# Kernel tuning notes

Measured on AMD Instinct MI355X. Metric: run time of the kernel, lower is better.

The kernel has to match this reference:

```python
import jax, jax.numpy as jnp
import numpy as np
from jax import lax

Z_MAX = 0.3
WAVELENGTHS = jnp.array([0.65, 0.53, 0.47], jnp.float32)
LUMA = jnp.array([0.299, 0.587, 0.114], jnp.float32)


def conv2d(x, w, b):
    # x: (B,C,H,W), w: (O,I,kh,kw), SAME padding, stride 1
    y = lax.conv_general_dilated(x, w, (1, 1), 'SAME',
                                 dimension_numbers=('NCHW', 'OIHW', 'NCHW'))
    return y + b[None, :, None, None]


def group_norm(x, g, b, eps=1e-5):
    # GroupNorm(num_groups=1): normalize over (C,H,W) per sample
    mu = x.mean(axis=(1, 2, 3), keepdims=True)
    var = ((x - mu) ** 2).mean(axis=(1, 2, 3), keepdims=True)
    xn = (x - mu) * lax.rsqrt(var + eps)
    return xn * g[None, :, None, None] + b[None, :, None, None]


def setup_inputs() -> dict:
    key = jax.random.key(0)
    ks = jax.random.split(key, 16)
    B, C, H, W = 8, 3, 512, 512
    PH, ZH, MH = 16, 16, 32
    s = 0.1
    inp = {
        'x': jax.random.uniform(ks[0], (B, C, H, W), jnp.float32),
        'norm_g': jnp.ones((C,), jnp.float32), 'norm_b': jnp.zeros((C,), jnp.float32),
        'ph_w1': jax.random.normal(ks[1], (PH, C, 3, 3), jnp.float32) * s,
        'ph_b1': jnp.zeros((PH,), jnp.float32),
        'ph_w2': jax.random.normal(ks[2], (C, PH, 3, 3), jnp.float32) * s,
        'ph_b2': jnp.zeros((C,), jnp.float32),
        'z_w1': jax.random.normal(ks[3], (ZH, C, 3, 3), jnp.float32) * s,
        'z_b1': jnp.zeros((ZH,), jnp.float32),
        'z_w2': jax.random.normal(ks[4], (C, ZH, 3, 3), jnp.float32) * s,
        'z_b2': jnp.zeros((C,), jnp.float32),
        'freq_gain': jax.random.normal(ks[5], (C,), jnp.float32) * 0.01,
        'mix_w1': jax.random.normal(ks[6], (MH, C + 2, 3, 3), jnp.float32) * s,
        'mix_b1': jnp.zeros((MH,), jnp.float32),
        'gn1_g': jnp.ones((MH,), jnp.float32), 'gn1_b': jnp.zeros((MH,), jnp.float32),
        'mix_w2': jax.random.normal(ks[7], (MH, MH, 3, 3), jnp.float32) * s,
        'mix_b2': jnp.zeros((MH,), jnp.float32),
        'gn2_g': jnp.ones((MH,), jnp.float32), 'gn2_b': jnp.zeros((MH,), jnp.float32),
        'mix_w3': jax.random.normal(ks[8], (C, MH, 1, 1), jnp.float32) * s,
        'mix_b3': jnp.zeros((C,), jnp.float32),
        'se_w1': jax.random.normal(ks[9], (4, C), jnp.float32) * s,   # mid = max(3//4,4)=4
        'se_b1': jnp.zeros((4,), jnp.float32),
        'se_w2': jax.random.normal(ks[10], (C, 4), jnp.float32) * s,
        'se_b2': jnp.zeros((C,), jnp.float32),
        'alpha': jnp.asarray(0.3, jnp.float32),
    }
    return inp


def reference(x, norm_g, norm_b, ph_w1, ph_b1, ph_w2, ph_b2,
              z_w1, z_b1, z_w2, z_b2, freq_gain,
              mix_w1, mix_b1, gn1_g, gn1_b, mix_w2, mix_b2, gn2_g, gn2_b,
              mix_w3, mix_b3, se_w1, se_b1, se_w2, se_b2, alpha):
    B, C, H, W = x.shape
    # 1) norm
    xn = group_norm(x, norm_g, norm_b)
    # 2) phase prediction (small CNN, phi in [-pi, pi])
    h = jax.nn.silu(conv2d(xn, ph_w1, ph_b1))
    phi = jnp.tanh(conv2d(h, ph_w2, ph_b2)) * jnp.pi
    # 3) per-pixel propagation distance z in [0, z_max]
    hz = jax.nn.silu(conv2d(xn, z_w1, z_b1))
    z = jax.nn.sigmoid(conv2d(hz, z_w2, z_b2)) * Z_MAX
    # 4) complex field U0 = amp * exp(i*phi)  (amp_mode='identity')
    U0 = lax.complex(x * jnp.cos(phi), x * jnp.sin(phi))
    # 5) ASM propagation. kz = 2*pi*sqrt(1/lam^2 - fx^2 - fy^2), per-channel wavelength.
    fy = jnp.fft.fftfreq(H).astype(jnp.float32)
    fx = jnp.fft.fftfreq(W).astype(jnp.float32)
    f2 = fy[:, None] ** 2 + fx[None, :] ** 2                     # (H,W)
    inv_l2 = (1.0 / WAVELENGTHS ** 2)[:, None, None]             # (3,1,1)
    kz = 2.0 * jnp.pi * jnp.sqrt(jnp.maximum(inv_l2 - f2[None], 0.0))  # (3,H,W)
    # spatially varying z: base propagation at mean z + spatial phase correction
    z_mean = z.mean(axis=(2, 3), keepdims=True)                  # (B,3,1,1)
    Uf = jnp.fft.fft2(U0)
    Uf = Uf * (1.0 + freq_gain)[None, :, None, None].astype(Uf.dtype)  # FreqEnhance gain
    hp = kz[None] * z_mean                                       # (B,3,H,W)
    Uz = jnp.fft.ifft2(Uf * lax.complex(jnp.cos(hp), jnp.sin(hp)))
    k0 = (2.0 * jnp.pi / WAVELENGTHS)[None, :, None, None]
    cp = k0 * (z - z_mean)
    Uz = Uz * lax.complex(jnp.cos(cp), jnp.sin(cp))
    # 6) J = |Uz| with clamped sqrt
    J = jnp.sqrt(jnp.maximum(Uz.real ** 2 + Uz.imag ** 2, 1e-12))
    # 7) mix head: [x, J_luma, J_contrast] -> delta
    lw = LUMA[None, :, None, None]
    x_l = (x * lw).sum(axis=1, keepdims=True)
    J_l = (J * lw).sum(axis=1, keepdims=True)
    mix_in = jnp.concatenate([x, J_l, J_l - x_l], axis=1)        # (B,5,H,W)
    d = jax.nn.silu(group_norm(conv2d(mix_in, mix_w1, mix_b1), gn1_g, gn1_b))
    d = jax.nn.silu(group_norm(conv2d(d, mix_w2, mix_b2), gn2_g, gn2_b))
    delta = conv2d(d, mix_w3, mix_b3)                            # (B,3,H,W)
    # 8) SE channel attention
    p = delta.mean(axis=(2, 3))                                  # (B,3)
    wse = jax.nn.sigmoid(jax.nn.silu(p @ se_w1.T + se_b1) @ se_w2.T + se_b2)
    delta = delta * wse[:, :, None, None]
    # 9) residual update
    return x + alpha * delta
```

## Files before the change

### kernel.cpp

```cpp
#include <hip/hip_runtime.h>
#include <hip/hip_bf16.h>
#include <math.h>

#define DINL __device__ __forceinline__

namespace {
constexpr int Bn = 8, Cn = 3, Hn = 512, Wn = 512;
constexpr int HW  = Hn * Wn;
constexpr int CHW = Cn * HW;
constexpr float GEPS = 1e-5f;
constexpr float PIf  = 3.14159265358979323846f;

constexpr size_t OFF_RED = 0;
constexpr size_t OFF_PHI = 512;
constexpr size_t OFF_U   = OFF_PHI + (size_t)Bn * CHW * 2;
constexpr size_t OFF_J   = OFF_U   + (size_t)Bn * CHW * 4;
constexpr size_t OFF_D   = OFF_J   + (size_t)Bn * CHW * 2;
constexpr size_t OFF_Y2  = OFF_D   + (size_t)Bn * CHW * 2;
constexpr size_t OFF_W1B = OFF_Y2  + (size_t)Bn * 32 * HW;
constexpr size_t OFF_W2F = OFF_W1B + 3072 * 2;
constexpr size_t OFF_WH1 = OFF_W2F + 9216;
constexpr size_t OFF_WP2 = OFF_WH1 + 4608 * 2;
constexpr size_t OFF_WZ2 = OFF_WP2 + 4608;
constexpr size_t OFF_PRM = OFF_WZ2 + 4608;
constexpr size_t OFF_PART= OFF_PRM + 160 * 4;
constexpr size_t OFF_TW  = OFF_PART + 81920 * 4;
constexpr int PZ = 0;
constexpr int PG1 = 24576;
constexpr int PG2 = 40960;
constexpr int PD  = 57344;
}

typedef __bf16 bfx8 __attribute__((ext_vector_type(8)));
typedef float  fx4  __attribute__((ext_vector_type(4)));
typedef float  fx2  __attribute__((ext_vector_type(2)));

DINL float frcp(float a) { return __builtin_amdgcn_rcpf(a); }
DINL float sigm(float a) { return frcp(1.f + __expf(-a)); }
DINL float siluf(float a) { return a * frcp(1.f + __expf(-a)); }
DINL float ftanh(float a) { return 1.f - 2.f * frcp(1.f + __expf(2.f * a)); }
DINL unsigned short f2bf(float f) {
    unsigned u = __float_as_uint(f);
    return (unsigned short)((u + 0x7FFFu + ((u >> 16) & 1u)) >> 16);
}
DINL float bf2f(unsigned short h) {
    return __uint_as_float(((unsigned)h) << 16);
}
DINL unsigned short t1(float a) { return (unsigned short)(__float_as_uint(a) >> 16); }
DINL unsigned t2(float a, float b) {
    return (__float_as_uint(a) >> 16) | (__float_as_uint(b) & 0xFFFF0000u);
}
DINL unsigned char f2f8(float v) {
    return (unsigned char)(__builtin_amdgcn_cvt_pk_fp8_f32(v, v, 0, false) & 0xFF);
}
DINL unsigned short pk8(float a, float b) {
    return (unsigned short)(__builtin_amdgcn_cvt_pk_fp8_f32(a, b, 0, false) & 0xFFFF);
}
DINL unsigned pk4f8(float a, float b, float c, float d) {
    unsigned u = __builtin_amdgcn_cvt_pk_fp8_f32(a, b, 0, false);
    u = __builtin_amdgcn_cvt_pk_fp8_f32(c, d, u, true);
    return u;
}
template<int SEL>
DINL float f8f(unsigned u) { return __builtin_amdgcn_cvt_f32_fp8(u, SEL); }
DINL unsigned pkh(float a, float b) {
    auto h = __builtin_amdgcn_cvt_pkrtz(a, b);
    unsigned u; __builtin_memcpy(&u, &h, 4); return u;
}
DINL float2 uph(unsigned u) {
    _Float16 h[2]; __builtin_memcpy(h, &u, 4);
    return make_float2((float)h[0], (float)h[1]);
}
DINL unsigned short f2h(float a) {
    _Float16 h = (_Float16)a; unsigned short s; __builtin_memcpy(&s, &h, 2); return s;
}
DINL float h2f(unsigned short s) {
    _Float16 h; __builtin_memcpy(&h, &s, 2); return (float)h;
}

DINL int SW(int e) { return e ^ ((e >> 4) & 7); }

DINL float blockReduceSum(float v) {
    __shared__ float sm[4];
    int lane = threadIdx.x & 63, wid = threadIdx.x >> 6;
    #pragma unroll
    for (int o = 32; o > 0; o >>= 1) v += __shfl_down(v, o, 64);
    __syncthreads();
    if (lane == 0) sm[wid] = v;
    __syncthreads();
    if (wid == 0) {
        float r = (lane < 4) ? sm[lane] : 0.f;
        r += __shfl_down(r, 2, 64);
        r += __shfl_down(r, 1, 64);
        return r;
    }
    return 0.f;
}

DINL void blockReduceSum3(float& a, float& b, float& c) {
    __shared__ float sm3[12];
    int lane = threadIdx.x & 63, wid = threadIdx.x >> 6;
    #pragma unroll
    for (int o = 32; o > 0; o >>= 1) {
        a += __shfl_down(a, o, 64);
        b += __shfl_down(b, o, 64);
        c += __shfl_down(c, o, 64);
    }
    __syncthreads();
    if (lane == 0) { sm3[wid] = a; sm3[4 + wid] = b; sm3[8 + wid] = c; }
    __syncthreads();
    if (threadIdx.x == 0) {
        a = sm3[0] + sm3[1] + sm3[2] + sm3[3];
        b = sm3[4] + sm3[5] + sm3[6] + sm3[7];
        c = sm3[8] + sm3[9] + sm3[10] + sm3[11];
    }
}

__global__ __launch_bounds__(256) void k_init(
    const float* __restrict__ w1, const float* __restrict__ w2,
    const float* __restrict__ phw1, const float* __restrict__ zw1,
    const float* __restrict__ phw2, const float* __restrict__ zw2,
    const float* __restrict__ g2g, const float* __restrict__ g2b,
    const float* __restrict__ w3,
    unsigned short* __restrict__ w1bf, unsigned char* __restrict__ w2f8,
    unsigned short* __restrict__ wh1, unsigned char* __restrict__ wp2,
    unsigned char* __restrict__ wz2, float* __restrict__ prm,
    float2* __restrict__ gtw,
    const float* __restrict__ x, float* __restrict__ part)
{
    if (blockIdx.x < 36) {
        int i = blockIdx.x * 256 + threadIdx.x;
        if (i < 3072) {
            int o = i / 96, k = i - o * 96;
            int ky = k >> 5, r = k & 31, kx = r >> 3, c = r & 7;
            float v = (kx < 3 && c < 5) ? w1[o * 45 + c * 9 + ky * 3 + kx] : 0.f;
            w1bf[i] = f2bf(v);
        }
        if (i < 9216) {
            int tap = i >> 10, rr = i & 1023, o = rr >> 5, ci = rr & 31;
            w2f8[i] = f2f8(w2[o * 288 + ci * 9 + tap]);
        }
        if (i < 4608) {
            int o = i / 96, k = i - o * 96;
            int ky = k >> 5, r = k & 31, kx = r >> 3, c = r & 7;
            float v = 0.f;
            if (kx < 3 && c < 3)
                v = (o < 16) ? phw1[o * 27 + c * 9 + ky * 3 + kx]
                             : zw1[(o - 16) * 27 + c * 9 + ky * 3 + kx];
            wh1[i] = f2bf(v);
        }
        if (i < 4608) {
            int tap = i / 512, rr = i - tap * 512, n = rr >> 5, k = rr & 31;
            float vp = (n < 3 && k < 16) ? phw2[n * 144 + k * 9 + tap] : 0.f;
            float vz = (n < 3) ? zw2[n * 288 + k * 9 + tap] : 0.f;
            wp2[i] = f2f8(vp);
            wz2[i] = f2f8(vz);
        }
        if (i < 160) {
            if (i < 32) {
                int ch = (i & 1) * 16 + (i >> 1);
                prm[i] = g2g[ch];
            } else if (i < 64) {
                int j = i - 32, ch = (j & 1) * 16 + (j >> 1);
                prm[i] = g2b[ch];
            } else {
                int j = (i - 64) & 31, c = (i - 64) >> 5;
                int ch = (j & 1) * 16 + (j >> 1);
                prm[i] = w3[c * 32 + ch];
            }
        }
        return;
    }
    if (blockIdx.x == 36) {
        for (int i = threadIdx.x; i < 512; i += 256) {
            float s, c; __sincosf(-2.f * PIf * (float)i * (1.f / 512.f), &s, &c);
            gtw[i] = make_float2(c, s);
        }
        return;
    }
    const int bid = blockIdx.x - 37;
    const int b = bid >> 5, blk = bid & 31;
    const float4* xv = (const float4*)(x + (size_t)b * CHW + (size_t)blk * (CHW / 32));
    float s = 0.f, ss = 0.f;
    for (int i = threadIdx.x; i < (CHW / 32) / 4; i += 256) {
        float4 v = xv[i];
        s  += v.x + v.y + v.z + v.w;
        ss += v.x * v.x + v.y * v.y + v.z * v.z + v.w * v.w;
    }
    float rs = blockReduceSum(s);
    float rss = blockReduceSum(ss);
    if (threadIdx.x == 0) {
        part[PG1 + b * 64 + blk] = rs;
        part[PG1 + b * 64 + 32 + blk] = rss;
    }
}

__global__ __launch_bounds__(256) void k_heads(
    const float* __restrict__ x,
    const float* __restrict__ ng, const float* __restrict__ nb,
    const unsigned short* __restrict__ wh1,
    const float* __restrict__ phb1, const float* __restrict__ zb1,
    const unsigned char* __restrict__ wp2, const unsigned char* __restrict__ wz2,
    const float* __restrict__ phb2, const float* __restrict__ zb2,
    unsigned short* __restrict__ phi, float* __restrict__ part)
{
    const int tx0 = blockIdx.x * 16, ty0 = blockIdx.y * 16, b = blockIdx.z;
    const int local = blockIdx.y * 32 + blockIdx.x;
    const bool edge = (blockIdx.x == 0) || (blockIdx.x == 31) ||
                      (blockIdx.y == 0) || (blockIdx.y == 31);
    __shared__ unsigned short mt8[20 * 21 * 8];
    __shared__ __attribute__((aligned(16))) unsigned char ht8[324 * 48];
    __shared__ float xst[2];
    const int t = threadIdx.x;
    {
        const float* px = part + PG1 + (size_t)b * 64;
        float sv  = (t < 32) ? px[t] : 0.f;
        float ssv = (t >= 32 && t < 64) ? px[t] : 0.f;
        float r0 = blockReduceSum(sv);
        float r1 = blockReduceSum(ssv);
        if (t == 0) { xst[0] = r0; xst[1] = r1; }
        __syncthreads();
    }
    const float mu = xst[0] * (1.f / CHW);
    const float rsv = rsqrtf(xst[1] * (1.f / CHW) - mu * mu + GEPS);
    float sc[3], sh[3];
    #pragma unroll
    for (int c = 0; c < 3; ++c) { sc[c] = rsv * ng[c]; sh[c] = nb[c] - mu * rsv * ng[c]; }
    if (edge) {
        for (int e = t; e < 20 * 21; e += 256) {
            int yy = e / 21, xx = e - yy * 21;
            int gy = ty0 - 2 + yy, gx = tx0 - 2 + xx;
            float v0 = 0, v1 = 0, v2 = 0;
            if (xx < 20 && (unsigned)gy < (unsigned)Hn && (unsigned)gx < (unsigned)Wn) {
                size_t p = (size_t)b * CHW + (size_t)gy * Wn + gx;
                v0 = x[p] * sc[0] + sh[0];
                v1 = x[p + HW] * sc[1] + sh[1];
                v2 = x[p + 2 * HW] * sc[2] + sh[2];
            }
            *(uint4*)(mt8 + e * 8) = make_uint4(t2(v0, v1), (unsigned)t1(v2), 0u, 0u);
        }
    } else {
        for (int e = t; e < 20 * 21; e += 256) {
            int yy = e / 21, xx = e - yy * 21;
            float v0 = 0, v1 = 0, v2 = 0;
            if (xx < 20) {
                size_t p = (size_t)b * CHW + (size_t)(ty0 - 2 + yy) * Wn + (tx0 - 2 + xx);
                v0 = x[p] * sc[0] + sh[0];
                v1 = x[p + HW] * sc[1] + sh[1];
                v2 = x[p + 2 * HW] * sc[2] + sh[2];
            }
            *(uint4*)(mt8 + e * 8) = make_uint4(t2(v0, v1), (unsigned)t1(v2), 0u, 0u);
        }
    }
    const int wv = t >> 6, lane = t & 63, ln = lane & 15, q = lane >> 4;
    bfx8 Bf[3][3];
    #pragma unroll
    for (int ks = 0; ks < 3; ++ks)
        #pragma unroll
        for (int nt = 0; nt < 3; ++nt)
            Bf[ks][nt] = *(const bfx8*)(wh1 + (nt * 16 + ln) * 96 + ks * 32 + q * 8);
    float bph[4], bz0[4], bz1[4];
    #pragma unroll
    for (int r = 0; r < 4; ++r) {
        int ch = q * 4 + r;
        bph[r] = phb1[ch]; bz0[r] = zb1[ch]; bz1[r] = zb1[16 + ch];
    }
    __syncthreads();
    for (int mt = wv; mt < 21; mt += 4) {
        int p = mt * 16 + ln; if (p > 323) p = 323;
        const int hy = p / 18, hx = p - hy * 18;
        fx4 a0 = {0,0,0,0}, a1 = {0,0,0,0}, a2 = {0,0,0,0};
        #pragma unroll
        for (int ks = 0; ks < 3; ++ks) {
            bfx8 A = *(const bfx8*)(mt8 + ((hy + ks) * 21 + hx + q) * 8);
            a0 = __builtin_amdgcn_mfma_f32_16x16x32_bf16(Bf[ks][0], A, a0, 0, 0, 0);
            a1 = __builtin_amdgcn_mfma_f32_16x16x32_bf16(Bf[ks][1], A, a1, 0, 0, 0);
            a2 = __builtin_amdgcn_mfma_f32_16x16x32_bf16(Bf[ks][2], A, a2, 0, 0, 0);
        }
        bool live = true;
        if (edge) {
            const int gy = ty0 - 1 + hy, gx = tx0 - 1 + hx;
            live = (unsigned)gy < (unsigned)Hn && (unsigned)gx < (unsigned)Wn;
        }
        unsigned d0 = pk4f8(siluf(a0[0] + bph[0]), siluf(a0[1] + bph[1]),
                            siluf(a0[2] + bph[2]), siluf(a0[3] + bph[3]));
        unsigned d1 = pk4f8(siluf(a1[0] + bz0[0]), siluf(a1[1] + bz0[1]),
                            siluf(a1[2] + bz0[2]), siluf(a1[3] + bz0[3]));
        unsigned d2 = pk4f8(siluf(a2[0] + bz1[0]), siluf(a2[1] + bz1[1]),
                            siluf(a2[2] + bz1[2]), siluf(a2[3] + bz1[3]));
        if (!live) { d0 = 0u; d1 = 0u; d2 = 0u; }
        unsigned* hp = (unsigned*)(ht8 + p * 48 + q * 4);
        hp[0] = d0; hp[4] = d1; hp[8] = d2;
    }
    __syncthreads();
    fx4 accp[4], accz[4];
    #pragma unroll
    for (int i = 0; i < 4; ++i) { accp[i] = fx4{0,0,0,0}; accz[i] = fx4{0,0,0,0}; }
    #pragma unroll
    for (int tap = 0; tap < 9; ++tap) {
        const int ky = tap / 3, kx = tap - ky * 3;
        long Bp = *(const long*)(wp2 + tap * 512 + ln * 32 + q * 8);
        long Bz = *(const long*)(wz2 + tap * 512 + ln * 32 + q * 8);
        #pragma unroll
        for (int i = 0; i < 4; ++i) {
            const int oy = wv * 4 + i;
            const unsigned char* ap = ht8 + ((oy + ky) * 18 + ln + kx) * 48;
            long Ap = *(const long*)(ap + q * 8);
            long Az = *(const long*)(ap + 16 + q * 8);
            accp[i] = __builtin_amdgcn_mfma_f32_16x16x32_fp8_fp8(Ap, Bp, accp[i], 0, 0, 0);
            accz[i] = __builtin_amdgcn_mfma_f32_16x16x32_fp8_fp8(Az, Bz, accz[i], 0, 0, 0);
        }
    }
    __syncthreads();
    float* phs = (float*)ht8;
    float* zs  = phs + 1024;
    if (ln < 3) {
        #pragma unroll
        for (int i = 0; i < 4; ++i)
            #pragma unroll
            for (int r = 0; r < 4; ++r) {
                int pl = (wv * 4 + i) * 16 + q * 4 + r;
                phs[pl * 4 + ln] = accp[i][r];
                zs [pl * 4 + ln] = accz[i][r];
            }
    }
    asm volatile("" ::: "memory");
    float4 pv = ((const float4*)phs)[t];
    float4 zv = ((const float4*)zs)[t];
    const int gy = ty0 + (t >> 4), gx = tx0 + (t & 15);
    size_t pp = (size_t)b * CHW + (size_t)gy * Wn + gx;
    phi[pp]          = f2h(ftanh(pv.x + phb2[0]) * PIf);
    phi[pp + HW]     = f2h(ftanh(pv.y + phb2[1]) * PIf);
    phi[pp + 2 * HW] = f2h(ftanh(pv.z + phb2[2]) * PIf);
    float z0 = sigm(zv.x + zb2[0]) * 0.3f;
    float z1 = sigm(zv.y + zb2[1]) * 0.3f;
    float z2 = sigm(zv.z + zb2[2]) * 0.3f;
    blockReduceSum3(z0, z1, z2);
    if (t == 0) {
        part[PZ + (size_t)(b * 3 + 0) * 1024 + local] = z0;
        part[PZ + (size_t)(b * 3 + 1) * 1024 + local] = z1;
        part[PZ + (size_t)(b * 3 + 2) * 1024 + local] = z2;
    }
}

template<bool INV>
DINL float2* fft512_wave4(float2* a, float2* b, const float2* tw, int l)
{
    float2* src = a; float2* dst = b;
    int s = 1;
    #pragma unroll
    for (int st = 0; st < 4; ++st) {
        #pragma unroll
        for (int h = 0; h < 2; ++h) {
            const int i = l + h * 64;
            const int q = i & (s - 1);
            const int sm = i - q;
            const int si = SW(i);
            float2 A = src[si], B = src[si + 128], C = src[si + 256], D = src[si + 384];
            float t0x = A.x + C.x, t0y = A.y + C.y;
            float t1x = A.x - C.x, t1y = A.y - C.y;
            float t2x = B.x + D.x, t2y = B.y + D.y;
            float t3x = B.x - D.x, t3y = B.y - D.y;
            float i3x = INV ? -t3y : t3y;
            float i3y = INV ? t3x : -t3x;
            float u0x = t0x + t2x, u0y = t0y + t2y;
            float u2x = t0x - t2x, u2y = t0y - t2y;
            float u1x = t1x + i3x, u1y = t1y + i3y;
            float u3x = t1x - i3x, u3y = t1y - i3y;
            float2 w1 = tw[SW(sm)], w2 = tw[SW(2 * sm)], w3 = tw[SW(3 * sm)];
            float w1y = INV ? -w1.y : w1.y;
            float w2y = INV ? -w2.y : w2.y;
            float w3y = INV ? -w3.y : w3.y;
            const int base = q + 4 * sm;
            dst[SW(base)]         = make_float2(u0x, u0y);
            dst[SW(base + s)]     = make_float2(u1x * w1.x - u1y * w1y, u1x * w1y + u1y * w1.x);
            dst[SW(base + 2 * s)] = make_float2(u2x * w2.x - u2y * w2y, u2x * w2y + u2y * w2.x);
            dst[SW(base + 3 * s)] = make_float2(u3x * w3.x - u3y * w3y, u3x * w3y + u3y * w3.x);
        }
        float2* tmp = src; src = dst; dst = tmp;
        s <<= 2;
        asm volatile("" ::: "memory");
    }
    #pragma unroll
    for (int h = 0; h < 4; ++h) {
        const int j = l + h * 64;
        const int sj = SW(j);
        float2 u = src[sj], v = src[sj + 256];
        dst[sj]       = make_float2(u.x + v.x, u.y + v.y);
        dst[sj + 256] = make_float2(u.x - v.x, u.y - v.y);
    }
    float2* tmp = src; src = dst; dst = tmp;
    asm volatile("" ::: "memory");
    return src;
}

__global__ __launch_bounds__(256) void k_fftA(
    const float* __restrict__ x, const unsigned short* __restrict__ phi,
    unsigned* __restrict__ U, const float2* __restrict__ gtw)
{
    __shared__ float2 buf[4][2][512];
    __shared__ float2 tw[512];
    const int t = threadIdx.x, wv = t >> 6, l = t & 63;
    #pragma unroll
    for (int i = t; i < 512; i += 256) tw[SW(i)] = gtw[i];
    __syncthreads();
    const size_t line = (size_t)blockIdx.x * 4 + wv;
    const float* xr = x + line * 512;
    const unsigned short* pr = phi + line * 512;
    float2* A = buf[wv][0];
    float2* B = buf[wv][1];
    #pragma unroll
    for (int i = l; i < 512; i += 64) {
        float s, c; __sincosf(h2f(pr[i]), &s, &c);
        float xv = xr[i];
        A[SW(i)] = make_float2(xv * c, xv * s);
    }
    asm volatile("" ::: "memory");
    float2* res = fft512_wave4<false>(A, B, tw, l);
    unsigned* Ur = U + line * 512;
    #pragma unroll
    for (int i = l; i < 512; i += 64) {
        float2 v = res[SW(i)];
        Ur[i] = pkh(v.x, v.y);
    }
}

__global__ __launch_bounds__(256) void k_transpose(unsigned* __restrict__ U,
                                                   const float* __restrict__ part,
                                                   float* __restrict__ red)
{
    const int img = blockIdx.y;
    if (blockIdx.x == 0) {
        float4 a4 = ((const float4*)(part + PZ + (size_t)img * 1024))[threadIdx.x];
        float r = blockReduceSum(a4.x + a4.y + a4.z + a4.w);
        if (threadIdx.x == 0) red[16 + img] = r;
    }
    int rem = blockIdx.x, ti = 0;
    while (rem >= 8 - ti) { rem -= 8 - ti; ++ti; }
    const int tj = ti + rem;
    unsigned* Ub = U + (size_t)img * HW;
    __shared__ unsigned ta[64][65];
    __shared__ unsigned tb[64][65];
    const int t = threadIdx.x;
    const int cc = t & 63, r0 = t >> 6;
    const int ar = ti * 64, ac = tj * 64;
    #pragma unroll
    for (int k = 0; k < 16; ++k) {
        int r = r0 + k * 4;
        ta[r][cc] = Ub[(size_t)(ar + r) * 512 + ac + cc];
    }
    if (ti != tj) {
        #pragma unroll
        for (int k = 0; k < 16; ++k) {
            int r = r0 + k * 4;
            tb[r][cc] = Ub[(size_t)(ac + r) * 512 + ar + cc];
        }
    }
    __syncthreads();
    #pragma unroll
    for (int k = 0; k < 16; ++k) {
        int r = r0 + k * 4;
        Ub[(size_t)(ac + r) * 512 + ar + cc] = ta[cc][r];
    }
    if (ti != tj) {
        #pragma unroll
        for (int k = 0; k < 16; ++k) {
            int r = r0 + k * 4;
            Ub[(size_t)(ar + r) * 512 + ac + cc] = tb[cc][r];
        }
    }
}

__global__ __launch_bounds__(256) void k_fftB(
    unsigned* __restrict__ U, const float* __restrict__ red,
    const float* __restrict__ fgain, const float2* __restrict__ gtw)
{
    __shared__ float2 buf[4][2][512];
    __shared__ float2 tw[512];
    const int t = threadIdx.x, wv = t >> 6, l = t & 63;
    #pragma unroll
    for (int i = t; i < 512; i += 256) tw[SW(i)] = gtw[i];
    const int line = blockIdx.x * 4 + wv;
    const int bc = line >> 9;
    const int fw = line & 511;
    const int c = bc % 3;
    const float zm = red[16 + bc] * (1.f / HW);
    __syncthreads();
    unsigned* Ur = U + (size_t)line * 512;
    float2* A = buf[wv][0];
    float2* B = buf[wv][1];
    #pragma unroll
    for (int i = l; i < 512; i += 64) A[SW(i)] = uph(Ur[i]);
    asm volatile("" ::: "memory");
    float2* res = fft512_wave4<false>(A, B, tw, l);
    const float gain = 1.f + fgain[c];
    const float lam  = (c == 0) ? 0.65f : (c == 1) ? 0.53f : 0.47f;
    const float il2  = 1.f / (lam * lam);
    const float fwv  = (float)(fw < 256 ? fw : fw - 512) * (1.f / 512.f);
    const float f2w  = fwv * fwv;
    #pragma unroll
    for (int i = l; i < 512; i += 64) {
        float fh = (float)(i < 256 ? i : i - 512) * (1.f / 512.f);
        float kz = 2.f * PIf * sqrtf(fmaxf(il2 - f2w - fh * fh, 0.f));
        float sn, cs; __sincosf(kz * zm, &sn, &cs);
        const int si = SW(i);
        float2 v = res[si];
        res[si] = make_float2(gain * (v.x * cs - v.y * sn), gain * (v.x * sn + v.y * cs));
    }
    asm volatile("" ::: "memory");
    float2* other = (res == A) ? B : A;
    float2* res2 = fft512_wave4<true>(res, other, tw, l);
    #pragma unroll
    for (int i = l; i < 512; i += 64) {
        float2 v = res2[SW(i)];
        Ur[i] = pkh(v.x * (1.f / 512.f), v.y * (1.f / 512.f));
    }
}

__global__ __launch_bounds__(256) void k_fftC(
    const unsigned* __restrict__ U, unsigned short* __restrict__ J,
    const float2* __restrict__ gtw)
{
    __shared__ float2 buf[4][2][512];
    __shared__ float2 tw[512];
    const int t = threadIdx.x, wv = t >> 6, l = t & 63;
    #pragma unroll
    for (int i = t; i < 512; i += 256) tw[SW(i)] = gtw[i];
    __syncthreads();
    const size_t line = (size_t)blockIdx.x * 4 + wv;
    const unsigned* Ur = U + line * 512;
    float2* A = buf[wv][0];
    float2* B = buf[wv][1];
    #pragma unroll
    for (int i = l; i < 512; i += 64) A[SW(i)] = uph(Ur[i]);
    asm volatile("" ::: "memory");
    float2* res = fft512_wave4<true>(A, B, tw, l);
    unsigned short* Jr = J + line * 512;
    #pragma unroll
    for (int i = l; i < 512; i += 64) {
        float2 v = res[SW(i)];
        float re = v.x * (1.f / 512.f), im = v.y * (1.f / 512.f);
        Jr[i] = f2h(sqrtf(fmaxf(re * re + im * im, 1e-12f)));
    }
}

__global__ __launch_bounds__(256) void k_m1(
    const float* __restrict__ x, const unsigned short* __restrict__ Jb,
    const unsigned short* __restrict__ w1bf, const float* __restrict__ b1,
    float* __restrict__ part)
{
    const int tx0 = blockIdx.x * 16, ty0 = blockIdx.y * 16, b = blockIdx.z;
    const int local = blockIdx.y * 32 + blockIdx.x;
    const bool edge = (blockIdx.x == 0) || (blockIdx.x == 31) ||
                      (blockIdx.y == 0) || (blockIdx.y == 31);
    __shared__ unsigned short mt8[18 * 19 * 8];
    const int t = threadIdx.x;
    for (int e = t; e < 18 * 19; e += 256) {
        int yy = e / 19, xx = e - yy * 19;
        int gy = ty0 - 1 + yy, gx = tx0 - 1 + xx;
        float v0 = 0, v1 = 0, v2 = 0, jl = 0, d5 = 0;
        bool ok = edge ? (xx < 18 && (unsigned)gy < (unsigned)Hn && (unsigned)gx < (unsigned)Wn)
                       : (xx < 18);
        if (ok) {
            size_t p = (size_t)b * CHW + (size_t)gy * Wn + gx;
            v0 = x[p]; v1 = x[p + HW]; v2 = x[p + 2 * HW];
            float j0 = h2f(Jb[p]), j1 = h2f(Jb[p + HW]), j2 = h2f(Jb[p + 2 * HW]);
            float xl = 0.299f * v0 + 0.587f * v1 + 0.114f * v2;
            jl = 0.299f * j0 + 0.587f * j1 + 0.114f * j2;
            d5 = jl - xl;
        }
        *(uint4*)(mt8 + e * 8) = make_uint4(t2(v0, v1), t2(v2, jl), (unsigned)t1(d5), 0u);
    }
    __syncthreads();
    const int wv = t >> 6, lane = t & 63, ln = lane & 15, q = lane >> 4;
    bfx8 Bf[3][2];
    #pragma unroll
    for (int ks = 0; ks < 3; ++ks)
        #pragma unroll
        for (int nt = 0; nt < 2; ++nt)
            Bf[ks][nt] = *(const bfx8*)(w1bf + (nt * 16 + ln) * 96 + ks * 32 + q * 8);
    const float b1v0 = b1[ln], b1v1 = b1[16 + ln];
    float s = 0.f, ss = 0.f;
    #pragma unroll
    for (int i = 0; i < 4; ++i) {
        const int oy = wv * 4 + i;
        fx4 a0 = {0.f, 0.f, 0.f, 0.f}, a1 = {0.f, 0.f, 0.f, 0.f};
        #pragma unroll
        for (int ks = 0; ks < 3; ++ks) {
            bfx8 A = *(const bfx8*)(mt8 + ((oy + ks) * 19 + ln + q) * 8);
            a0 = __builtin_amdgcn_mfma_f32_16x16x32_bf16(A, Bf[ks][0], a0, 0, 0, 0);
            a1 = __builtin_amdgcn_mfma_f32_16x16x32_bf16(A, Bf[ks][1], a1, 0, 0, 0);
        }
        #pragma unroll
        for (int r = 0; r < 4; ++r) {
            float u0 = a0[r] + b1v0, u1 = a1[r] + b1v1;
            s += u0 + u1; ss += u0 * u0 + u1 * u1;
        }
    }
    float rs = blockReduceSum(s);
    float rss = blockReduceSum(ss);
    if (t == 0) {
        part[PG1 + (size_t)b * 1024 + local] = rs;
        part[PG1 + (size_t)(8 + b) * 1024 + local] = rss;
    }
}

__global__ __launch_bounds__(256) void k_m2(
    const float* __restrict__ x, const unsigned short* __restrict__ Jb,
    const unsigned short* __restrict__ w1bf, const float* __restrict__ b1,
    const float* __restrict__ g1g, const float* __restrict__ g1b,
    const unsigned char* __restrict__ w2f8, const float* __restrict__ b2,
    float* __restrict__ part, unsigned char* __restrict__ y2)
{
    const int tx0 = blockIdx.x * 16, ty0 = blockIdx.y * 16, b = blockIdx.z;
    const int local = blockIdx.y * 32 + blockIdx.x;
    const bool edge = (blockIdx.x == 0) || (blockIdx.x == 31) ||
                      (blockIdx.y == 0) || (blockIdx.y == 31);
    __shared__ unsigned short mt8[20 * 21 * 8];
    __shared__ __attribute__((aligned(16))) unsigned char dt2[324 * 40];
    __shared__ float g1s[2];
    const int t = threadIdx.x;
    {
        float4 a4 = ((const float4*)(part + PG1 + (size_t)b * 1024))[t];
        float4 c4 = ((const float4*)(part + PG1 + (size_t)(8 + b) * 1024))[t];
        float r0 = blockReduceSum(a4.x + a4.y + a4.z + a4.w);
        float r1 = blockReduceSum(c4.x + c4.y + c4.z + c4.w);
        if (t == 0) { g1s[0] = r0; g1s[1] = r1; }
        __syncthreads();
    }
    const float mu1 = g1s[0] * (1.f / (32.f * HW));
    const float rs1 = rsqrtf(g1s[1] * (1.f / (32.f * HW)) - mu1 * mu1 + GEPS);
    for (int e = t; e < 20 * 21; e += 256) {
        int yy = e / 21, xx = e - yy * 21;
        int gy = ty0 - 2 + yy, gx = tx0 - 2 + xx;
        float v0 = 0, v1 = 0, v2 = 0, jl = 0, d5 = 0;
        bool ok = edge ? (xx < 20 && (unsigned)gy < (unsigned)Hn && (unsigned)gx < (unsigned)Wn)
                       : (xx < 20);
        if (ok) {
            size_t p = (size_t)b * CHW + (size_t)gy * Wn + gx;
            v0 = x[p]; v1 = x[p + HW]; v2 = x[p + 2 * HW];
            float j0 = h2f(Jb[p]), j1 = h2f(Jb[p + HW]), j2 = h2f(Jb[p + 2 * HW]);
            float xl = 0.299f * v0 + 0.587f * v1 + 0.114f * v2;
            jl = 0.299f * j0 + 0.587f * j1 + 0.114f * j2;
            d5 = jl - xl;
        }
        *(uint4*)(mt8 + e * 8) = make_uint4(t2(v0, v1), t2(v2, jl), (unsigned)t1(d5), 0u);
    }
    const int wv = t >> 6, lane = t & 63, ln = lane & 15, q = lane >> 4;
    float scv[2][4], ofv[2][4];
    #pragma unroll
    for (int g = 0; g < 2; ++g)
        #pragma unroll
        for (int r = 0; r < 4; ++r) {
            int ch = g * 16 + q * 4 + r;
            float sg = rs1 * g1g[ch];
            scv[g][r] = sg;
            ofv[g][r] = (b1[ch] - mu1) * sg + g1b[ch];
        }
    bfx8 Bf[3][2];
    #pragma unroll
    for (int ks = 0; ks < 3; ++ks)
        #pragma unroll
        for (int nt = 0; nt < 2; ++nt)
            Bf[ks][nt] = *(const bfx8*)(w1bf + (nt * 16 + ln) * 96 + ks * 32 + q * 8);
    __syncthreads();
    for (int mt = wv; mt < 21; mt += 4) {
        int p = mt * 16 + ln; if (p > 323) p = 323;
        const int hy = p / 18, hx = p - hy * 18;
        fx4 a0 = {0.f, 0.f, 0.f, 0.f}, a1 = {0.f, 0.f, 0.f, 0.f};
        #pragma unroll
        for (int ks = 0; ks < 3; ++ks) {
            bfx8 A = *(const bfx8*)(mt8 + ((hy + ks) * 21 + hx + q) * 8);
            a0 = __builtin_amdgcn_mfma_f32_16x16x32_bf16(Bf[ks][0], A, a0, 0, 0, 0);
            a1 = __builtin_amdgcn_mfma_f32_16x16x32_bf16(Bf[ks][1], A, a1, 0, 0, 0);
        }
        bool live = true;
        if (edge) {
            const int gy = ty0 - 1 + hy, gx = tx0 - 1 + hx;
            live = (unsigned)gy < (unsigned)Hn && (unsigned)gx < (unsigned)Wn;
        }
        unsigned d0 = pk4f8(siluf(a0[0] * scv[0][0] + ofv[0][0]),
                            siluf(a0[1] * scv[0][1] + ofv[0][1]),
                            siluf(a0[2] * scv[0][2] + ofv[0][2]),
                            siluf(a0[3] * scv[0][3] + ofv[0][3]));
        unsigned d1 = pk4f8(siluf(a1[0] * scv[1][0] + ofv[1][0]),
                            siluf(a1[1] * scv[1][1] + ofv[1][1]),
                            siluf(a1[2] * scv[1][2] + ofv[1][2]),
                            siluf(a1[3] * scv[1][3] + ofv[1][3]));
        if (!live) { d0 = 0u; d1 = 0u; }
        unsigned* dp = (unsigned*)(dt2 + p * 40 + q * 4);
        dp[0] = d0; dp[4] = d1;
    }
    __syncthreads();
    fx4 c2[4][2];
    #pragma unroll
    for (int i = 0; i < 4; ++i)
        #pragma unroll
        for (int nt = 0; nt < 2; ++nt)
            c2[i][nt] = fx4{0.f, 0.f, 0.f, 0.f};
    #pragma unroll
    for (int tap = 0; tap < 9; ++tap) {
        const int ky = tap / 3, kx = tap - ky * 3;
        long B0 = *(const long*)(w2f8 + tap * 1024 + ln * 32 + q * 8);
        long B1 = *(const long*)(w2f8 + tap * 1024 + (16 + ln) * 32 + q * 8);
        #pragma unroll
        for (int i = 0; i < 4; ++i) {
            const int oy = wv * 4 + i;
            long A = *(const long*)(dt2 + ((oy + ky) * 18 + ln + kx) * 40 + q * 8);
            c2[i][0] = __builtin_amdgcn_mfma_f32_16x16x32_fp8_fp8(A, B0, c2[i][0], 0, 0, 0);
            c2[i][1] = __builtin_amdgcn_mfma_f32_16x16x32_fp8_fp8(A, B1, c2[i][1], 0, 0, 0);
        }
    }
    float s = 0.f, ss = 0.f;
    const float b2v0 = b2[ln], b2v1 = b2[16 + ln];
    #pragma unroll
    for (int i = 0; i < 4; ++i) {
        const int gy = ty0 + wv * 4 + i;
        #pragma unroll
        for (int r = 0; r < 4; ++r) {
            const int gx = tx0 + q * 4 + r;
            float a0 = c2[i][0][r] + b2v0;
            float a1 = c2[i][1][r] + b2v1;
            s += a0 + a1; ss += a0 * a0 + a1 * a1;
            size_t off = ((size_t)b * HW + (size_t)gy * Wn + gx) * 32 + ln * 2;
            *(unsigned short*)(y2 + off) = pk8(a0, a1);
        }
    }
    float rsum = blockReduceSum(s);
    float rss = blockReduceSum(ss);
    if (t == 0) {
        part[PG2 + (size_t)b * 1024 + local] = rsum;
        part[PG2 + (size_t)(8 + b) * 1024 + local] = rss;
    }
}

__global__ __launch_bounds__(256) void k_m3(
    const unsigned char* __restrict__ y2,
    const float* __restrict__ prm, const float* __restrict__ b3,
    unsigned short* __restrict__ dl, float* __restrict__ part)
{
    const int t = threadIdx.x;
    const int b = blockIdx.x >> 7;
    const int local = blockIdx.x & 127;
    __shared__ float g2s[2];
    __shared__ float lut[8192];
    {
        float4 a4 = ((const float4*)(part + PG2 + (size_t)b * 1024))[t];
        float4 c4 = ((const float4*)(part + PG2 + (size_t)(8 + b) * 1024))[t];
        float r0 = blockReduceSum(a4.x + a4.y + a4.z + a4.w);
        float r1 = blockReduceSum(c4.x + c4.y + c4.z + c4.w);
        if (t == 0) { g2s[0] = r0; g2s[1] = r1; }
        __syncthreads();
    }
    const float mu = g2s[0] * (1.f / (32.f * HW));
    const float rs = rsqrtf(g2s[1] * (1.f / (32.f * HW)) - mu * mu + GEPS);
    for (int e = t; e < 8192; e += 256) {
        int j = e >> 8;
        float v = f8f<0>((unsigned)(e & 255));
        lut[e] = siluf((v - mu) * rs * prm[j] + prm[32 + j]);
    }
    __syncthreads();
    const float bb0 = b3[0], bb1 = b3[1], bb2 = b3[2];
    float s0 = 0.f, s1 = 0.f, s2 = 0.f;
    #pragma unroll
    for (int k = 0; k < 8; ++k) {
        int idx = blockIdx.x * 2048 + k * 256 + t;
        int pix = idx & (HW - 1);
        const uint4* yp = (const uint4*)(y2 + (size_t)idx * 32);
        uint4 L0 = yp[0], L1 = yp[1];
        unsigned Lw[8] = {L0.x, L0.y, L0.z, L0.w, L1.x, L1.y, L1.z, L1.w};
        float a0 = bb0, a1 = bb1, a2 = bb2;
        #pragma unroll
        for (int w = 0; w < 8; ++w) {
            unsigned u = Lw[w];
            #pragma unroll
            for (int h = 0; h < 4; ++h) {
                int j = w * 4 + h;
                int code = (int)((u >> (8 * h)) & 255u);
                float sv = lut[j * 256 + code];
                a0 += sv * prm[64 + j]; a1 += sv * prm[96 + j]; a2 += sv * prm[128 + j];
            }
        }
        size_t p = (size_t)b * CHW + pix;
        dl[p] = f2h(a0); dl[p + HW] = f2h(a1); dl[p + 2 * HW] = f2h(a2);
        s0 += a0; s1 += a1; s2 += a2;
    }
    blockReduceSum3(s0, s1, s2);
    if (t == 0) {
        part[PD + (size_t)(b * 3 + 0) * 1024 + local] = s0;
        part[PD + (size_t)(b * 3 + 1) * 1024 + local] = s1;
        part[PD + (size_t)(b * 3 + 2) * 1024 + local] = s2;
    }
}

__global__ __launch_bounds__(256) void k_fin(
    const float* __restrict__ part, float* __restrict__ red,
    const float* __restrict__ w1, const float* __restrict__ b1,
    const float* __restrict__ w2, const float* __restrict__ b2,
    const float* __restrict__ alpha)
{
    __shared__ float sm[24];
    const int t = threadIdx.x, wv = t >> 6, l = t & 63;
    for (int g = wv; g < 24; g += 4) {
        const float* p = part + PD + (size_t)g * 1024;
        float s = p[l] + p[l + 64];
        #pragma unroll
        for (int o = 32; o > 0; o >>= 1) s += __shfl_down(s, o, 64);
        if (l == 0) sm[g] = s;
    }
    __syncthreads();
    if (t < 8) {
        int b = t;
        float p0 = sm[b * 3 + 0] * (1.f / HW);
        float p1 = sm[b * 3 + 1] * (1.f / HW);
        float p2 = sm[b * 3 + 2] * (1.f / HW);
        float h[4];
        #pragma unroll
        for (int j = 0; j < 4; ++j) {
            float a = b1[j] + p0 * w1[j * 3] + p1 * w1[j * 3 + 1] + p2 * w1[j * 3 + 2];
            h[j] = siluf(a);
        }
        float al = alpha[0];
        #pragma unroll
        for (int c = 0; c < 3; ++c) {
            float a = b2[c] + h[0] * w2[c * 4] + h[1] * w2[c * 4 + 1]
                            + h[2] * w2[c * 4 + 2] + h[3] * w2[c * 4 + 3];
            red[96 + b * 3 + c] = al * sigm(a);
        }
    }
}

__global__ __launch_bounds__(256) void k_out(
    const float* __restrict__ x, const unsigned short* __restrict__ dl,
    const float* __restrict__ red, float* __restrict__ out)
{
    int i = blockIdx.x * 256 + threadIdx.x;
    float aw = red[96 + (i >> 16)];
    float4 xv = ((const float4*)x)[i];
    uint2 dv2 = ((const uint2*)dl)[i];
    float2 d01 = uph(dv2.x);
    float2 d23 = uph(dv2.y);
    float4 o;
    o.x = xv.x + aw * d01.x; o.y = xv.y + aw * d01.y;
    o.z = xv.z + aw * d23.x; o.w = xv.w + aw * d23.y;
    ((float4*)out)[i] = o;
}

extern "C" void kernel_launch(void* const* d_in, const int* in_sizes, int n_in,
                              void* d_out, int out_size, void* d_ws, size_t ws_size,
                              hipStream_t stream)
{
    const float* x     = (const float*)d_in[0];
    const float* ng    = (const float*)d_in[1];
    const float* nb    = (const float*)d_in[2];
    const float* ph_w1 = (const float*)d_in[3];
    const float* ph_b1 = (const float*)d_in[4];
    const float* ph_w2 = (const float*)d_in[5];
    const float* ph_b2 = (const float*)d_in[6];
    const float* z_w1  = (const float*)d_in[7];
    const float* z_b1  = (const float*)d_in[8];
    const float* z_w2  = (const float*)d_in[9];
    const float* z_b2  = (const float*)d_in[10];
    const float* fgain = (const float*)d_in[11];
    const float* mw1   = (const float*)d_in[12];
    const float* mb1   = (const float*)d_in[13];
    const float* g1g   = (const float*)d_in[14];
    const float* g1b   = (const float*)d_in[15];
    const float* mw2   = (const float*)d_in[16];
    const float* mb2   = (const float*)d_in[17];
    const float* g2g   = (const float*)d_in[18];
    const float* g2b   = (const float*)d_in[19];
    const float* mw3   = (const float*)d_in[20];
    const float* mb3   = (const float*)d_in[21];
    const float* sw1   = (const float*)d_in[22];
    const float* sb1   = (const float*)d_in[23];
    const float* sw2   = (const float*)d_in[24];
    const float* sb2   = (const float*)d_in[25];
    const float* alpha = (const float*)d_in[26];

    char* ws = (char*)d_ws;
    float*  red = (float*)(ws + OFF_RED);
    unsigned short* phi = (unsigned short*)(ws + OFF_PHI);
    unsigned* U = (unsigned*)(ws + OFF_U);
    unsigned short* Jb = (unsigned short*)(ws + OFF_J);
    unsigned short* dl = (unsigned short*)(ws + OFF_D);
    unsigned char*  y2   = (unsigned char*)(ws + OFF_Y2);
    unsigned short* w1bf = (unsigned short*)(ws + OFF_W1B);
    unsigned char*  w2f8 = (unsigned char*)(ws + OFF_W2F);
    unsigned short* wh1  = (unsigned short*)(ws + OFF_WH1);
    unsigned char*  wp2  = (unsigned char*)(ws + OFF_WP2);
    unsigned char*  wz2  = (unsigned char*)(ws + OFF_WZ2);
    float* prm  = (float*)(ws + OFF_PRM);
    float* part = (float*)(ws + OFF_PART);
    float2* gtw = (float2*)(ws + OFF_TW);
    float* out = (float*)d_out;

    hipLaunchKernelGGL(k_init, dim3(293), dim3(256), 0, stream,
                       mw1, mw2, ph_w1, z_w1, ph_w2, z_w2, g2g, g2b, mw3,
                       w1bf, w2f8, wh1, wp2, wz2, prm, gtw, x, part);
    hipLaunchKernelGGL(k_heads, dim3(32, 32, 8), dim3(256), 0, stream,
                       x, ng, nb, wh1, ph_b1, z_b1, wp2, wz2, ph_b2, z_b2, phi, part);
    hipLaunchKernelGGL(k_fftA, dim3(3072), dim3(256), 0, stream, x, phi, U, gtw);
    hipLaunchKernelGGL(k_transpose, dim3(36, 24), dim3(256), 0, stream, U, part, red);
    hipLaunchKernelGGL(k_fftB, dim3(3072), dim3(256), 0, stream, U, red, fgain, gtw);
    hipLaunchKernelGGL(k_transpose, dim3(36, 24), dim3(256), 0, stream, U, part, red);
    hipLaunchKernelGGL(k_fftC, dim3(3072), dim3(256), 0, stream, U, Jb, gtw);
    hipLaunchKernelGGL(k_m1, dim3(32, 32, 8), dim3(256), 0, stream, x, Jb, w1bf, mb1, part);
    hipLaunchKernelGGL(k_m2, dim3(32, 32, 8), dim3(256), 0, stream,
                       x, Jb, w1bf, mb1, g1g, g1b, w2f8, mb2, part, y2);
    hipLaunchKernelGGL(k_m3, dim3(1024), dim3(256), 0, stream, y2, prm, mb3, dl, part);
    hipLaunchKernelGGL(k_fin, dim3(1), dim3(256), 0, stream, part, red, sw1, sb1, sw2, sb2, alpha);
    hipLaunchKernelGGL(k_out, dim3(6144), dim3(256), 0, stream, x, dl, red, out);
}
```

Measured before the change: 462.1 us.

## Fold luma-difference channel into conv weights, retile m1, swap MFMA operands for packed stores

Folds the J_l - x_l input channel into the first mix conv weights so the 5-channel input shrinks to 4 and the per-pixel x-luma and difference math goes away. k_m1 now uses 32x32 tiles with a 34x35 halo, which lowers halo overhead and block count, and k_m2 reads only the 256 resulting partials. The heads and m2 kernels swap MFMA A/B operands so each lane holds consecutive output channels, which allows packed 4-byte fp8 stores into y2 and changes the channel ordering in prm. This risks layout mismatches in downstream consumers such as k_m3, which is not shown here.

```diff
diff --git a/kernel.cpp b/kernel.cpp
--- a/kernel.cpp
+++ b/kernel.cpp
@@ -133,7 +133,13 @@
         if (i < 3072) {
             int o = i / 96, k = i - o * 96;
             int ky = k >> 5, r = k & 31, kx = r >> 3, c = r & 7;
-            float v = (kx < 3 && c < 5) ? w1[o * 45 + c * 9 + ky * 3 + kx] : 0.f;
+            float v = 0.f;
+            if (kx < 3 && c < 4) {
+                float base = w1[o * 45 + c * 9 + ky * 3 + kx];
+                float w4   = w1[o * 45 + 4 * 9 + ky * 3 + kx];
+                v = (c == 3) ? base + w4
+                  : base - ((c == 0) ? 0.299f : (c == 1) ? 0.587f : 0.114f) * w4;
+            }
             w1bf[i] = f2bf(v);
         }
         if (i < 9216) {
@@ -158,15 +164,12 @@
         }
         if (i < 160) {
             if (i < 32) {
-                int ch = (i & 1) * 16 + (i >> 1);
-                prm[i] = g2g[ch];
+                prm[i] = g2g[i];
             } else if (i < 64) {
-                int j = i - 32, ch = (j & 1) * 16 + (j >> 1);
-                prm[i] = g2b[ch];
+                prm[i] = g2b[i - 32];
             } else {
                 int j = (i - 64) & 31, c = (i - 64) >> 5;
-                int ch = (j & 1) * 16 + (j >> 1);
-                prm[i] = w3[c * 32 + ch];
+                prm[i] = w3[c * 32 + j];
             }
         }
         return;
@@ -307,22 +310,23 @@
             const unsigned char* ap = ht8 + ((oy + ky) * 18 + ln + kx) * 48;
             long Ap = *(const long*)(ap + q * 8);
             long Az = *(const long*)(ap + 16 + q * 8);
-            accp[i] = __builtin_amdgcn_mfma_f32_16x16x32_fp8_fp8(Ap, Bp, accp[i], 0, 0, 0);
-            accz[i] = __builtin_amdgcn_mfma_f32_16x16x32_fp8_fp8(Az, Bz, accz[i], 0, 0, 0);
+            accp[i] = __builtin_amdgcn_mfma_f32_16x16x32_fp8_fp8(Bp, Ap, accp[i], 0, 0, 0);
+            accz[i] = __builtin_amdgcn_mfma_f32_16x16x32_fp8_fp8(Bz, Az, accz[i], 0, 0, 0);
         }
     }
     __syncthreads();
     float* phs = (float*)ht8;
     float* zs  = phs + 1024;
-    if (ln < 3) {
-        #pragma unroll
-        for (int i = 0; i < 4; ++i)
+    if (q == 0) {
+        #pragma unroll
+        for (int i = 0; i < 4; ++i) {
+            int pl = (wv * 4 + i) * 16 + ln;
             #pragma unroll
-            for (int r = 0; r < 4; ++r) {
-                int pl = (wv * 4 + i) * 16 + q * 4 + r;
-                phs[pl * 4 + ln] = accp[i][r];
-                zs [pl * 4 + ln] = accz[i][r];
+            for (int r = 0; r < 3; ++r) {
+                phs[pl * 4 + r] = accp[i][r];
+                zs [pl * 4 + r] = accz[i][r];
             }
+        }
     }
     asm volatile("" ::: "memory");
     float4 pv = ((const float4*)phs)[t];
@@ -549,27 +553,24 @@
     const unsigned short* __restrict__ w1bf, const float* __restrict__ b1,
     float* __restrict__ part)
 {
-    const int tx0 = blockIdx.x * 16, ty0 = blockIdx.y * 16, b = blockIdx.z;
-    const int local = blockIdx.y * 32 + blockIdx.x;
-    const bool edge = (blockIdx.x == 0) || (blockIdx.x == 31) ||
-                      (blockIdx.y == 0) || (blockIdx.y == 31);
-    __shared__ unsigned short mt8[18 * 19 * 8];
+    const int tx0 = blockIdx.x * 32, ty0 = blockIdx.y * 32, b = blockIdx.z;
+    const int local = blockIdx.y * 16 + blockIdx.x;
+    const bool edge = (blockIdx.x == 0) || (blockIdx.x == 15) ||
+                      (blockIdx.y == 0) || (blockIdx.y == 15);
+    __shared__ unsigned short mt8[34 * 35 * 8];
     const int t = threadIdx.x;
-    for (int e = t; e < 18 * 19; e += 256) {
-        int yy = e / 19, xx = e - yy * 19;
+    for (int e = t; e < 34 * 35; e += 256) {
+        int yy = e / 35, xx = e - yy * 35;
         int gy = ty0 - 1 + yy, gx = tx0 - 1 + xx;
-        float v0 = 0, v1 = 0, v2 = 0, jl = 0, d5 = 0;
-        bool ok = edge ? (xx < 18 && (unsigned)gy < (unsigned)Hn && (unsigned)gx < (unsigned)Wn)
-                       : (xx < 18);
+        float v0 = 0, v1 = 0, v2 = 0, jl = 0;
+        bool ok = edge ? (xx < 34 && (unsigned)gy < (unsigned)Hn && (unsigned)gx < (unsigned)Wn)
+                       : (xx < 34);
         if (ok) {
             size_t p = (size_t)b * CHW + (size_t)gy * Wn + gx;
             v0 = x[p]; v1 = x[p + HW]; v2 = x[p + 2 * HW];
-            float j0 = h2f(Jb[p]), j1 = h2f(Jb[p + HW]), j2 = h2f(Jb[p + 2 * HW]);
-            float xl = 0.299f * v0 + 0.587f * v1 + 0.114f * v2;
-            jl = 0.299f * j0 + 0.587f * j1 + 0.114f * j2;
-            d5 = jl - xl;
-        }
-        *(uint4*)(mt8 + e * 8) = make_uint4(t2(v0, v1), t2(v2, jl), (unsigned)t1(d5), 0u);
+            jl = 0.299f * h2f(Jb[p]) + 0.587f * h2f(Jb[p + HW]) + 0.114f * h2f(Jb[p + 2 * HW]);
+        }
+        *(uint4*)(mt8 + e * 8) = make_uint4(t2(v0, v1), t2(v2, jl), 0u, 0u);
     }
     __syncthreads();
     const int wv = t >> 6, lane = t & 63, ln = lane & 15, q = lane >> 4;
@@ -581,13 +582,12 @@
             Bf[ks][nt] = *(const bfx8*)(w1bf + (nt * 16 + ln) * 96 + ks * 32 + q * 8);
     const float b1v0 = b1[ln], b1v1 = b1[16 + ln];
     float s = 0.f, ss = 0.f;
-    #pragma unroll
-    for (int i = 0; i < 4; ++i) {
-        const int oy = wv * 4 + i;
+    for (int g = wv; g < 64; g += 4) {
+        const int row = g >> 1, ct = (g & 1) * 16;
         fx4 a0 = {0.f, 0.f, 0.f, 0.f}, a1 = {0.f, 0.f, 0.f, 0.f};
         #pragma unroll
         for (int ks = 0; ks < 3; ++ks) {
-            bfx8 A = *(const bfx8*)(mt8 + ((oy + ks) * 19 + ln + q) * 8);
+            bfx8 A = *(const bfx8*)(mt8 + ((row + ks) * 35 + ct + ln + q) * 8);
             a0 = __builtin_amdgcn_mfma_f32_16x16x32_bf16(A, Bf[ks][0], a0, 0, 0, 0);
             a1 = __builtin_amdgcn_mfma_f32_16x16x32_bf16(A, Bf[ks][1], a1, 0, 0, 0);
         }
@@ -621,10 +621,13 @@
     __shared__ float g1s[2];
     const int t = threadIdx.x;
     {
-        float4 a4 = ((const float4*)(part + PG1 + (size_t)b * 1024))[t];
-        float4 c4 = ((const float4*)(part + PG1 + (size_t)(8 + b) * 1024))[t];
+        float4 a4 = make_float4(0.f, 0.f, 0.f, 0.f), c4v = a4;
+        if (t < 64) {
+            a4  = ((const float4*)(part + PG1 + (size_t)b * 1024))[t];
+            c4v = ((const float4*)(part + PG1 + (size_t)(8 + b) * 1024))[t];
+        }
         float r0 = blockReduceSum(a4.x + a4.y + a4.z + a4.w);
-        float r1 = blockReduceSum(c4.x + c4.y + c4.z + c4.w);
+        float r1 = blockReduceSum(c4v.x + c4v.y + c4v.z + c4v.w);
         if (t == 0) { g1s[0] = r0; g1s[1] = r1; }
         __syncthreads();
     }
@@ -633,18 +636,15 @@
     for (int e = t; e < 20 * 21; e += 256) {
         int yy = e / 21, xx = e - yy * 21;
         int gy = ty0 - 2 + yy, gx = tx0 - 2 + xx;
-        float v0 = 0, v1 = 0, v2 = 0, jl = 0, d5 = 0;
+        float v0 = 0, v1 = 0, v2 = 0, jl = 0;
         bool ok = edge ? (xx < 20 && (unsigned)gy < (unsigned)Hn && (unsigned)gx < (unsigned)Wn)
                        : (xx < 20);
         if (ok) {
             size_t p = (size_t)b * CHW + (size_t)gy * Wn + gx;
             v0 = x[p]; v1 = x[p + HW]; v2 = x[p + 2 * HW];
-            float j0 = h2f(Jb[p]), j1 = h2f(Jb[p + HW]), j2 = h2f(Jb[p + 2 * HW]);
-            float xl = 0.299f * v0 + 0.587f * v1 + 0.114f * v2;
-            jl = 0.299f * j0 + 0.587f * j1 + 0.114f * j2;
-            d5 = jl - xl;
-        }
-        *(uint4*)(mt8 + e * 8) = make_uint4(t2(v0, v1), t2(v2, jl), (unsigned)t1(d5), 0u);
+            jl = 0.299f * h2f(Jb[p]) + 0.587f * h2f(Jb[p + HW]) + 0.114f * h2f(Jb[p + 2 * HW]);
+        }
+        *(uint4*)(mt8 + e * 8) = make_uint4(t2(v0, v1), t2(v2, jl), 0u, 0u);
     }
     const int wv = t >> 6, lane = t & 63, ln = lane & 15, q = lane >> 4;
     float scv[2][4], ofv[2][4];
@@ -707,24 +707,31 @@
         for (int i = 0; i < 4; ++i) {
             const int oy = wv * 4 + i;
             long A = *(const long*)(dt2 + ((oy + ky) * 18 + ln + kx) * 40 + q * 8);
-            c2[i][0] = __builtin_amdgcn_mfma_f32_16x16x32_fp8_fp8(A, B0, c2[i][0], 0, 0, 0);
-            c2[i][1] = __builtin_amdgcn_mfma_f32_16x16x32_fp8_fp8(A, B1, c2[i][1], 0, 0, 0);
-        }
-    }
+            c2[i][0] = __builtin_amdgcn_mfma_f32_16x16x32_fp8_fp8(B0, A, c2[i][0], 0, 0, 0);
+            c2[i][1] = __builtin_amdgcn_mfma_f32_16x16x32_fp8_fp8(B1, A, c2[i][1], 0, 0, 0);
+        }
+    }
+    float bv[2][4];
+    #pragma unroll
+    for (int nt = 0; nt < 2; ++nt)
+        #pragma unroll
+        for (int r = 0; r < 4; ++r)
+            bv[nt][r] = b2[nt * 16 + q * 4 + r];
     float s = 0.f, ss = 0.f;
-    const float b2v0 = b2[ln], b2v1 = b2[16 + ln];
+    const int gxo = tx0 + ln;
     #pragma unroll
     for (int i = 0; i < 4; ++i) {
         const int gy = ty0 + wv * 4 + i;
-        #pragma unroll
-        for (int r = 0; r < 4; ++r) {
-            const int gx = tx0 + q * 4 + r;
-            float a0 = c2[i][0][r] + b2v0;
-            float a1 = c2[i][1][r] + b2v1;
-            s += a0 + a1; ss += a0 * a0 + a1 * a1;
-            size_t off = ((size_t)b * HW + (size_t)gy * Wn + gx) * 32 + ln * 2;
-            *(unsigned short*)(y2 + off) = pk8(a0, a1);
-        }
+        size_t base = ((size_t)b * HW + (size_t)gy * Wn + gxo) * 32 + q * 4;
+        float v0 = c2[i][0][0] + bv[0][0], v1 = c2[i][0][1] + bv[0][1];
+        float v2 = c2[i][0][2] + bv[0][2], v3 = c2[i][0][3] + bv[0][3];
+        float w0 = c2[i][1][0] + bv[1][0], w1 = c2[i][1][1] + bv[1][1];
+        float w2 = c2[i][1][2] + bv[1][2], w3 = c2[i][1][3] + bv[1][3];
+        s  += v0 + v1 + v2 + v3 + w0 + w1 + w2 + w3;
+        ss += v0 * v0 + v1 * v1 + v2 * v2 + v3 * v3
+            + w0 * w0 + w1 * w1 + w2 * w2 + w3 * w3;
+        *(unsigned*)(y2 + base)      = pk4f8(v0, v1, v2, v3);
+        *(unsigned*)(y2 + base + 16) = pk4f8(w0, w1, w2, w3);
     }
     float rsum = blockReduceSum(s);
     float rss = blockReduceSum(ss);
@@ -905,7 +912,7 @@
     hipLaunchKernelGGL(k_fftB, dim3(3072), dim3(256), 0, stream, U, red, fgain, gtw);
     hipLaunchKernelGGL(k_transpose, dim3(36, 24), dim3(256), 0, stream, U, part, red);
     hipLaunchKernelGGL(k_fftC, dim3(3072), dim3(256), 0, stream, U, Jb, gtw);
-    hipLaunchKernelGGL(k_m1, dim3(32, 32, 8), dim3(256), 0, stream, x, Jb, w1bf, mb1, part);
+    hipLaunchKernelGGL(k_m1, dim3(16, 16, 8), dim3(256), 0, stream, x, Jb, w1bf, mb1, part);
     hipLaunchKernelGGL(k_m2, dim3(32, 32, 8), dim3(256), 0, stream,
                        x, Jb, w1bf, mb1, g1g, g1b, w2f8, mb2, part, y2);
     hipLaunchKernelGGL(k_m3, dim3(1024), dim3(256), 0, stream, y2, prm, mb3, dl, part);
```

Result: slower. 476.7 us (+3.2%).
